# Performance work log

Measured on AMD Instinct MI355X. Metric: run time of the kernel, lower is better.

## Reference

```python
import jax, jax.numpy as jnp
import numpy as np

N_NODES = 100_000
N_EDGES = 1_600_000
NUM_BASIS = 10
MAX_RADIUS = 5.0
NUM_NEIGHBORS = 10.0


def _sph_harm_lmax2(u):
    # u: [E,3] unit vectors. e3nn real spherical harmonics, lmax=2,
    # normalization='component' (each l-block has per-component unit variance).
    x, y, z = u[:, 0], u[:, 1], u[:, 2]
    s3 = jnp.sqrt(3.0)
    s5 = jnp.sqrt(5.0)
    s15 = jnp.sqrt(15.0)
    return jnp.stack([
        jnp.ones_like(x),                      # l=0
        s3 * x, s3 * y, s3 * z,                # l=1
        s15 * x * z,                           # l=2
        s15 * x * y,
        s5 * (y * y - 0.5 * (x * x + z * z)),
        s15 * y * z,
        0.5 * s15 * (z * z - x * x),
    ], axis=-1)                                # [E,9]


def _soft_one_hot_smooth_finite(r):
    # e3nn soft_one_hot_linspace(r, 0, max_radius, num_basis, 'smooth_finite', cutoff=True)
    vals = jnp.linspace(0.0, MAX_RADIUS, NUM_BASIS + 2)
    step = vals[1] - vals[0]
    vals = vals[1:-1]
    d = (r[:, None] - vals[None, :]) / step    # [E,num_basis]
    inside = jnp.abs(d) < 1.0
    d2 = jnp.where(inside, d * d, 0.0)
    y = 1.14136 * jnp.exp(2.0) * jnp.exp(-1.0 / (1.0 - d2))
    return jnp.where(inside, y, 0.0)


def setup_inputs() -> dict:
    key = jax.random.key(0)
    k1, k2, k3, k4, k5, k6 = jax.random.split(key, 6)
    return {
        "pos": jax.random.normal(k1, (N_NODES, 3), dtype=jnp.float32),
        "node_feats": jax.random.normal(k2, (N_NODES, 9), dtype=jnp.float32),
        "W1": jax.random.normal(k3, (NUM_BASIS, 16), dtype=jnp.float32),
        "W2": jax.random.normal(k4, (16, 3), dtype=jnp.float32),
        "edge_src": jax.random.randint(k5, (N_EDGES,), 0, N_NODES, dtype=jnp.int32),
        "edge_dst": jax.random.randint(k6, (N_EDGES,), 0, N_NODES, dtype=jnp.int32),
    }


def reference(pos, node_feats, W1, W2, edge_src, edge_dst):
    # gather: per-edge geometry
    edge_vec = pos[edge_dst] - pos[edge_src]          # [E,3]
    r = jnp.linalg.norm(edge_vec, axis=-1)            # [E]
    u = edge_vec / (r[:, None] + 1e-12)
    sh = _sph_harm_lmax2(u)                           # [E,9]

    # radial embedding -> small MLP -> per-edge tensor-product weights (weight_numel=3)
    emb = _soft_one_hot_smooth_finite(r) * jnp.sqrt(jnp.float32(NUM_BASIS))
    h = jax.nn.relu(emb @ W1 / jnp.sqrt(jnp.float32(NUM_BASIS))) * jnp.sqrt(2.0)
    w = h @ W2 / jnp.sqrt(16.0)                       # [E,3]

    # FullyConnectedTensorProduct('1x0e+1x1o+1x2e', sh, '1x0e'), shared_weights=False
    # paths: 0e*0e->0e, 1o*1o->0e, 2e*2e->0e ; w3j(l,l,0)=I/sqrt(2l+1); fan-in 3 paths.
    x1 = node_feats[edge_src]                         # [E,9]
    path_s = x1[:, 0] * sh[:, 0]
    path_p = jnp.sum(x1[:, 1:4] * sh[:, 1:4], axis=-1) / jnp.sqrt(3.0)
    path_d = jnp.sum(x1[:, 4:9] * sh[:, 4:9], axis=-1) / jnp.sqrt(5.0)
    msg = (w[:, 0] * path_s + w[:, 1] * path_p + w[:, 2] * path_d) / jnp.sqrt(3.0)

    # scatter-aggregate messages to destination nodes
    node_out = jax.ops.segment_sum(msg, edge_dst, num_segments=N_NODES)
    node_out = node_out / jnp.sqrt(jnp.float32(NUM_NEIGHBORS))
    return node_out[:, None]                          # [N,1] scalar ('1x0e') per node
```

## Files before the change

kernel.cpp:

```cpp
#include <hip/hip_runtime.h>
#include <math.h>

#define N_NODES 100000
#define N_EDGES 1600000

#define BUCKETS 8
#define GSPLIT 32
#define BUCKET_NODES (N_NODES / BUCKETS)
#define NSEG (BUCKETS * GSPLIT)
#define CAP 8192
#define CPAD 32

typedef _Float16 half8 __attribute__((ext_vector_type(8)));
typedef _Float16 half4 __attribute__((ext_vector_type(4)));

__global__ __launch_bounds__(256) void pack_kernel(
    const float* __restrict__ pos,
    const float* __restrict__ feats,
    half8* __restrict__ srcw,
    half4* __restrict__ posh,
    int*   __restrict__ counters)
{
    const int i = blockIdx.x * blockDim.x + threadIdx.x;
    if (blockIdx.x == 0) {
        for (int c = threadIdx.x; c < NSEG * CPAD; c += 256) counters[c] = 0;
    }
    if (i >= N_NODES) return;
    const float* p = pos + 3 * i;
    const float* f = feats + 9 * i;
    half8 a, b;
    a[0] = (_Float16)p[0]; a[1] = (_Float16)p[1]; a[2] = (_Float16)p[2];
    a[3] = (_Float16)f[0]; a[4] = (_Float16)f[1]; a[5] = (_Float16)f[2];
    a[6] = (_Float16)f[3]; a[7] = (_Float16)f[4];
    b[0] = (_Float16)f[5]; b[1] = (_Float16)f[6]; b[2] = (_Float16)f[7];
    b[3] = (_Float16)f[8]; b[4] = (_Float16)0; b[5] = (_Float16)0;
    b[6] = (_Float16)0;    b[7] = (_Float16)0;
    srcw[2 * i + 0] = a;
    srcw[2 * i + 1] = b;
    half4 q;
    q[0] = (_Float16)p[0]; q[1] = (_Float16)p[1]; q[2] = (_Float16)p[2];
    q[3] = (_Float16)0;
    posh[i] = q;
}

__device__ __forceinline__ float edge_msg_h(
    const half8 ra, const half8 rb, const half4 pd,
    const float* __restrict__ sW1, const float* __restrict__ sW2)
{
    const float vx = (float)pd[0] - (float)ra[0];
    const float vy = (float)pd[1] - (float)ra[1];
    const float vz = (float)pd[2] - (float)ra[2];

    const float r   = sqrtf(vx * vx + vy * vy + vz * vz);
    const float inv = 1.0f / (r + 1e-12f);
    const float x = vx * inv, y = vy * inv, z = vz * inv;

    const float s3  = 1.7320508075688772f;
    const float s5  = 2.23606797749979f;
    const float s15 = 3.872983346207417f;
    const float sh1 = s3 * x;
    const float sh2 = s3 * y;
    const float sh3 = s3 * z;
    const float sh4 = s15 * x * z;
    const float sh5 = s15 * x * y;
    const float sh6 = s5 * (y * y - 0.5f * (x * x + z * z));
    const float sh7 = s15 * y * z;
    const float sh8 = 0.5f * s15 * (z * z - x * x);

    const float q = r * 2.2f;
    const int   k = (int)floorf(q);
    int   b0 = k - 1, b1 = k;
    const float d0 = q - (float)k;
    const float d1 = d0 - 1.0f;
    const float A = 8.43357307f;
    float e0 = 0.0f, e1 = 0.0f;
    if (b0 >= 0 && b0 < 10) {
        const float dd = d0 * d0;
        if (dd < 1.0f) e0 = A * expf(-1.0f / (1.0f - dd));
    }
    if (b1 >= 0 && b1 < 10) {
        const float dd = d1 * d1;
        if (dd < 1.0f) e1 = A * expf(-1.0f / (1.0f - dd));
    }
    b0 = (b0 >= 0 && b0 < 10) ? b0 : 0;
    b1 = (b1 >= 0 && b1 < 10) ? b1 : 0;

    const float* w1r0 = sW1 + b0 * 17;
    const float* w1r1 = sW1 + b1 * 17;
    float acc0 = 0.0f, acc1 = 0.0f, acc2 = 0.0f;
#pragma unroll
    for (int j = 0; j < 16; ++j) {
        const float hj = fmaxf(e0 * w1r0[j] + e1 * w1r1[j], 0.0f);
        acc0 = fmaf(hj, sW2[j * 3 + 0], acc0);
        acc1 = fmaf(hj, sW2[j * 3 + 1], acc1);
        acc2 = fmaf(hj, sW2[j * 3 + 2], acc2);
    }

    const float path_s = (float)ra[3];
    const float path_p = ((float)ra[4] * sh1 + (float)ra[5] * sh2
                        + (float)ra[6] * sh3) * 0.5773502691896258f;
    const float path_d = ((float)ra[7] * sh4 + (float)rb[0] * sh5
                        + (float)rb[1] * sh6 + (float)rb[2] * sh7
                        + (float)rb[3] * sh8) * 0.4472135954999579f;

    const float FINAL = 0.06454972243679028f;
    return (acc0 * path_s + acc1 * path_p + acc2 * path_d) * FINAL;
}

__global__ __launch_bounds__(256) void msg_part_kernel(
    const half8* __restrict__ srcw,
    const half4* __restrict__ posh,
    const float* __restrict__ W1,
    const float* __restrict__ W2,
    const int* __restrict__ edge_src,
    const int* __restrict__ edge_dst,
    int*  __restrict__ counters,
    int2* __restrict__ segs)
{
    __shared__ float sW1[10 * 17];
    __shared__ float sW2[16 * 3];
    __shared__ int cnt[BUCKETS];
    __shared__ int basesm[BUCKETS];
    const int t = threadIdx.x;
    if (t < 160) sW1[(t >> 4) * 17 + (t & 15)] = W1[t];
    if (t < 48)  sW2[t] = W2[t];
    if (t < BUCKETS) cnt[t] = 0;
    __syncthreads();

    const int e = blockIdx.x * 256 + t;
    const int s = edge_src[e];
    const int d = edge_dst[e];
    const half8 ra = srcw[2 * s + 0];
    const half8 rb = srcw[2 * s + 1];
    const half4 pd = posh[d];
    const float m = edge_msg_h(ra, rb, pd, sW1, sW2);

    const int mybucket = d / BUCKET_NODES;
    const int local    = d - mybucket * BUCKET_NODES;
    const int rank = atomicAdd(&cnt[mybucket], 1);
    __syncthreads();

    const int g = blockIdx.x & (GSPLIT - 1);
    if (t < BUCKETS)
        basesm[t] = atomicAdd(&counters[(t * GSPLIT + g) * CPAD], cnt[t]);
    __syncthreads();

    const int slot = basesm[mybucket] + rank;
    if (slot < CAP)
        segs[(size_t)(mybucket * GSPLIT + g) * CAP + slot] =
            make_int2(local, __float_as_int(m));
}

__global__ __launch_bounds__(256) void scatter_kernel(
    const int* __restrict__ counters,
    const int2* __restrict__ segs,
    float* __restrict__ slabs)
{
    __shared__ float acc[BUCKET_NODES];
    const int seg = blockIdx.x;
    const int t = threadIdx.x;
    for (int i = t; i < BUCKET_NODES; i += 256) acc[i] = 0.0f;
    __syncthreads();

    int count = counters[seg * CPAD];
    if (count > CAP) count = CAP;
    const int2* sp = segs + (size_t)seg * CAP;
    for (int i = t; i < count; i += 256) {
        const int2 pr = sp[i];
        atomicAdd(&acc[pr.x], __int_as_float(pr.y));
    }
    __syncthreads();

    float* slab = slabs + (size_t)seg * BUCKET_NODES;
    for (int i = t; i < BUCKET_NODES; i += 256) slab[i] = acc[i];
}

__global__ __launch_bounds__(256) void reduce_kernel(
    const float* __restrict__ slabs, float* __restrict__ out)
{
    const int n = blockIdx.x * blockDim.x + threadIdx.x;
    if (n >= N_NODES) return;
    const int b = n / BUCKET_NODES;
    const int i = n - b * BUCKET_NODES;
    const float* sl = slabs + ((size_t)b * GSPLIT) * BUCKET_NODES + i;
    float sum = 0.0f;
#pragma unroll
    for (int g = 0; g < GSPLIT; ++g) sum += sl[(size_t)g * BUCKET_NODES];
    out[n] = sum;
}

__global__ __launch_bounds__(256) void edge_kernel_direct(
    const float* __restrict__ pos,
    const float* __restrict__ node_feats,
    const float* __restrict__ W1,
    const float* __restrict__ W2,
    const int*   __restrict__ edge_src,
    const int*   __restrict__ edge_dst,
    float* __restrict__ out)
{
    __shared__ float sW1[10 * 17];
    __shared__ float sW2[16 * 3];
    const int t = threadIdx.x;
    if (t < 160) sW1[(t >> 4) * 17 + (t & 15)] = W1[t];
    if (t < 48)  sW2[t] = W2[t];
    __syncthreads();

    const int e = blockIdx.x * blockDim.x + t;
    if (e >= N_EDGES) return;

    const int src = edge_src[e];
    const int dst = edge_dst[e];
    const float* ps = pos + 3 * src;
    const float* pdp = pos + 3 * dst;
    const float* xf = node_feats + 9 * src;
    half8 ra, rb; half4 pd;
    ra[0] = (_Float16)ps[0]; ra[1] = (_Float16)ps[1]; ra[2] = (_Float16)ps[2];
    ra[3] = (_Float16)xf[0]; ra[4] = (_Float16)xf[1]; ra[5] = (_Float16)xf[2];
    ra[6] = (_Float16)xf[3]; ra[7] = (_Float16)xf[4];
    rb[0] = (_Float16)xf[5]; rb[1] = (_Float16)xf[6]; rb[2] = (_Float16)xf[7];
    rb[3] = (_Float16)xf[8]; rb[4] = rb[5] = rb[6] = rb[7] = (_Float16)0;
    pd[0] = (_Float16)pdp[0]; pd[1] = (_Float16)pdp[1]; pd[2] = (_Float16)pdp[2];
    pd[3] = (_Float16)0;
    const float m = edge_msg_h(ra, rb, pd, sW1, sW2);
    unsafeAtomicAdd(out + dst, m);
}

extern "C" void kernel_launch(void* const* d_in, const int* in_sizes, int n_in,
                              void* d_out, int out_size, void* d_ws, size_t ws_size,
                              hipStream_t stream) {
    const float* pos        = (const float*)d_in[0];
    const float* node_feats = (const float*)d_in[1];
    const float* W1         = (const float*)d_in[2];
    const float* W2         = (const float*)d_in[3];
    const int*   edge_src   = (const int*)d_in[4];
    const int*   edge_dst   = (const int*)d_in[5];
    float* out = (float*)d_out;

    const size_t srcw_bytes = (size_t)N_NODES * 2 * sizeof(half8);
    const size_t posh_bytes = (size_t)N_NODES * sizeof(half4);
    const size_t cnt_bytes  = (size_t)NSEG * CPAD * sizeof(int);
    const size_t seg_bytes  = (size_t)NSEG * CAP * sizeof(int2);
    const size_t slab_bytes = (size_t)NSEG * BUCKET_NODES * sizeof(float);
    const size_t need = srcw_bytes + posh_bytes + cnt_bytes + seg_bytes + slab_bytes;

    if (ws_size >= need) {
        char* w = (char*)d_ws;
        half8* srcw  = (half8*)w;  w += srcw_bytes;
        half4* posh  = (half4*)w;  w += posh_bytes;
        int*   cnts  = (int*)w;    w += cnt_bytes;
        int2*  segs  = (int2*)w;   w += seg_bytes;
        float* slabs = (float*)w;

        pack_kernel<<<(N_NODES + 255) / 256, 256, 0, stream>>>(
            pos, node_feats, srcw, posh, cnts);
        msg_part_kernel<<<N_EDGES / 256, 256, 0, stream>>>(
            srcw, posh, W1, W2, edge_src, edge_dst, cnts, segs);
        scatter_kernel<<<NSEG, 256, 0, stream>>>(cnts, segs, slabs);
        reduce_kernel<<<(N_NODES + 255) / 256, 256, 0, stream>>>(slabs, out);
    } else {
        hipMemsetAsync(out, 0, N_NODES * sizeof(float), stream);
        edge_kernel_direct<<<(N_EDGES + 255) / 256, 256, 0, stream>>>(
            pos, node_feats, W1, W2, edge_src, edge_dst, out);
    }
}
```

Before: 122.2 us.

## Pack bucket entries into 32-bit (16-bit index + fp16 msg), rebalance buckets, two edges per thread

Each partitioned entry shrinks from an int2 (index plus fp32 message) to one 32-bit word holding a 16-bit local node index and an fp16 message. This halves the write traffic of the message kernel and the read traffic of the scatter kernel. The split changes to 16 buckets by 16 groups so that local indices fit in 16 bits and the shared accumulator per block is smaller, and each thread now handles two edges so the block-level atomics and syncs are amortised. The cost is fp16 rounding of each message before accumulation, which adds error. With twice as many edges per block and per bucket segment, the per-segment capacity of 8192 may also overflow and silently drop entries.

```diff
diff --git a/kernel.cpp b/kernel.cpp
--- a/kernel.cpp
+++ b/kernel.cpp
@@ -4,15 +4,29 @@
 #define N_NODES 100000
 #define N_EDGES 1600000
 
-#define BUCKETS 8
-#define GSPLIT 32
+#define BUCKETS 16
+#define GSPLIT 16
 #define BUCKET_NODES (N_NODES / BUCKETS)
 #define NSEG (BUCKETS * GSPLIT)
 #define CAP 8192
 #define CPAD 32
+#define EPB 512
 
 typedef _Float16 half8 __attribute__((ext_vector_type(8)));
 typedef _Float16 half4 __attribute__((ext_vector_type(4)));
+
+__device__ __forceinline__ unsigned int pack_entry(int local, float m) {
+    _Float16 h = (_Float16)m;
+    unsigned short u;
+    __builtin_memcpy(&u, &h, 2);
+    return ((unsigned int)local << 16) | u;
+}
+__device__ __forceinline__ float entry_msg(unsigned int e) {
+    unsigned short u = (unsigned short)(e & 0xFFFFu);
+    _Float16 h;
+    __builtin_memcpy(&h, &u, 2);
+    return (float)h;
+}
 
 __global__ __launch_bounds__(256) void pack_kernel(
     const float* __restrict__ pos,
@@ -115,7 +129,7 @@
     const int* __restrict__ edge_src,
     const int* __restrict__ edge_dst,
     int*  __restrict__ counters,
-    int2* __restrict__ segs)
+    unsigned int* __restrict__ segs)
 {
     __shared__ float sW1[10 * 17];
     __shared__ float sW2[16 * 3];
@@ -127,17 +141,31 @@
     if (t < BUCKETS) cnt[t] = 0;
     __syncthreads();
 
-    const int e = blockIdx.x * 256 + t;
-    const int s = edge_src[e];
-    const int d = edge_dst[e];
-    const half8 ra = srcw[2 * s + 0];
-    const half8 rb = srcw[2 * s + 1];
-    const half4 pd = posh[d];
-    const float m = edge_msg_h(ra, rb, pd, sW1, sW2);
-
-    const int mybucket = d / BUCKET_NODES;
-    const int local    = d - mybucket * BUCKET_NODES;
-    const int rank = atomicAdd(&cnt[mybucket], 1);
+    const int e0 = blockIdx.x * EPB + t;
+    const int e1 = e0 + 256;
+
+    const int s0 = edge_src[e0];
+    const int d0 = edge_dst[e0];
+    const int s1 = edge_src[e1];
+    const int d1 = edge_dst[e1];
+
+    const half8 ra0 = srcw[2 * s0 + 0];
+    const half8 rb0 = srcw[2 * s0 + 1];
+    const half4 pd0 = posh[d0];
+    const half8 ra1 = srcw[2 * s1 + 0];
+    const half8 rb1 = srcw[2 * s1 + 1];
+    const half4 pd1 = posh[d1];
+
+    const float m0 = edge_msg_h(ra0, rb0, pd0, sW1, sW2);
+    const float m1 = edge_msg_h(ra1, rb1, pd1, sW1, sW2);
+
+    const int bk0 = d0 / BUCKET_NODES;
+    const int lo0 = d0 - bk0 * BUCKET_NODES;
+    const int bk1 = d1 / BUCKET_NODES;
+    const int lo1 = d1 - bk1 * BUCKET_NODES;
+
+    const int rank0 = atomicAdd(&cnt[bk0], 1);
+    const int rank1 = atomicAdd(&cnt[bk1], 1);
     __syncthreads();
 
     const int g = blockIdx.x & (GSPLIT - 1);
@@ -145,15 +173,17 @@
         basesm[t] = atomicAdd(&counters[(t * GSPLIT + g) * CPAD], cnt[t]);
     __syncthreads();
 
-    const int slot = basesm[mybucket] + rank;
-    if (slot < CAP)
-        segs[(size_t)(mybucket * GSPLIT + g) * CAP + slot] =
-            make_int2(local, __float_as_int(m));
+    const int slot0 = basesm[bk0] + rank0;
+    if (slot0 < CAP)
+        segs[(size_t)(bk0 * GSPLIT + g) * CAP + slot0] = pack_entry(lo0, m0);
+    const int slot1 = basesm[bk1] + rank1;
+    if (slot1 < CAP)
+        segs[(size_t)(bk1 * GSPLIT + g) * CAP + slot1] = pack_entry(lo1, m1);
 }
 
 __global__ __launch_bounds__(256) void scatter_kernel(
     const int* __restrict__ counters,
-    const int2* __restrict__ segs,
+    const unsigned int* __restrict__ segs,
     float* __restrict__ slabs)
 {
     __shared__ float acc[BUCKET_NODES];
@@ -164,10 +194,10 @@
 
     int count = counters[seg * CPAD];
     if (count > CAP) count = CAP;
-    const int2* sp = segs + (size_t)seg * CAP;
+    const unsigned int* sp = segs + (size_t)seg * CAP;
     for (int i = t; i < count; i += 256) {
-        const int2 pr = sp[i];
-        atomicAdd(&acc[pr.x], __int_as_float(pr.y));
+        const unsigned int pr = sp[i];
+        atomicAdd(&acc[pr >> 16], entry_msg(pr));
     }
     __syncthreads();
 
@@ -239,21 +269,21 @@
     const size_t srcw_bytes = (size_t)N_NODES * 2 * sizeof(half8);
     const size_t posh_bytes = (size_t)N_NODES * sizeof(half4);
     const size_t cnt_bytes  = (size_t)NSEG * CPAD * sizeof(int);
-    const size_t seg_bytes  = (size_t)NSEG * CAP * sizeof(int2);
+    const size_t seg_bytes  = (size_t)NSEG * CAP * sizeof(unsigned int);
     const size_t slab_bytes = (size_t)NSEG * BUCKET_NODES * sizeof(float);
     const size_t need = srcw_bytes + posh_bytes + cnt_bytes + seg_bytes + slab_bytes;
 
     if (ws_size >= need) {
         char* w = (char*)d_ws;
-        half8* srcw  = (half8*)w;  w += srcw_bytes;
-        half4* posh  = (half4*)w;  w += posh_bytes;
-        int*   cnts  = (int*)w;    w += cnt_bytes;
-        int2*  segs  = (int2*)w;   w += seg_bytes;
+        half8* srcw  = (half8*)w;        w += srcw_bytes;
+        half4* posh  = (half4*)w;        w += posh_bytes;
+        int*   cnts  = (int*)w;          w += cnt_bytes;
+        unsigned int* segs = (unsigned int*)w;  w += seg_bytes;
         float* slabs = (float*)w;
 
         pack_kernel<<<(N_NODES + 255) / 256, 256, 0, stream>>>(
             pos, node_feats, srcw, posh, cnts);
-        msg_part_kernel<<<N_EDGES / 256, 256, 0, stream>>>(
+        msg_part_kernel<<<N_EDGES / EPB, 256, 0, stream>>>(
             srcw, posh, W1, W2, edge_src, edge_dst, cnts, segs);
         scatter_kernel<<<NSEG, 256, 0, stream>>>(cnts, segs, slabs);
         reduce_kernel<<<(N_NODES + 255) / 256, 256, 0, stream>>>(slabs, out);
```

Result: no change. 123.4 us (+0.9%).
